# Optimization experiments

Measured on AMD Instinct MI355X. Metric: run time of the kernel, lower is better.

The kernel has to match this reference:

```python
import jax, jax.numpy as jnp
from jax import lax
import numpy as np
import math

T, B, F = 512, 256, 256  # num_steps, batch, input_size == hidden_size
H = F


def setup_inputs() -> dict:
    key = jax.random.key(0)
    ks = jax.random.split(key, 20)
    stdv = 1.0 / math.sqrt(H)

    def u(k, n):
        return jax.random.uniform(k, (n,), jnp.float32, -stdv, stdv)

    X = jax.random.normal(ks[0], (T, B, F), jnp.float32)
    Mask = (jax.random.uniform(ks[1], (T, B, F)) < 0.7).astype(jnp.float32)
    Delta = jax.random.uniform(ks[2], (T, B, F), jnp.float32)

    return {
        "X": X, "Mask": Mask, "Delta": Delta,
        "x_mean": u(ks[3], F),
        "w_dg_x": u(ks[4], F), "b_dg_x": u(ks[5], F),
        "w_dg_h": u(ks[6], H), "b_dg_h": u(ks[7], H),
        "w_xz": u(ks[8], F), "u_hz": u(ks[9], H), "b_z": u(ks[10], H),
        "w_xr": u(ks[11], F), "u_hr": u(ks[12], H), "b_r": u(ks[13], H),
        "w_xh": u(ks[14], F), "u_hh": u(ks[15], H), "v_mh": u(ks[16], F),
        "b_h": u(ks[17], H),
    }


def reference(X, Mask, Delta, x_mean, w_dg_x, b_dg_x, w_dg_h, b_dg_h,
              w_xz, u_hz, b_z, w_xr, u_hr, b_r, w_xh, u_hh, v_mh, b_h):
    batch = X.shape[1]

    def step(h, inp):
        x, m, d = inp  # each [B, F]
        gamma_x = jnp.exp(-jnp.maximum(0.0, w_dg_x * d + b_dg_x))
        gamma_h = jnp.exp(-jnp.maximum(0.0, w_dg_h * d + b_dg_h))
        x = m * x + (1.0 - m) * (gamma_x * x + (1.0 - gamma_x) * x_mean)
        h = gamma_h * h
        z = jax.nn.sigmoid(w_xz * x + u_hz * h + b_z)
        r = jax.nn.sigmoid(w_xr * x + u_hr * h + b_r)
        h_tilde = jnp.tanh(w_xh * x + u_hh * (r * h) + v_mh * m + b_h)
        h = (1.0 - z) * h + z * h_tilde
        return h, h

    h0 = jnp.zeros((batch, H), X.dtype)
    _, hs = lax.scan(step, h0, (X, Mask, Delta))  # hs: [T, B, H]
    hidden_states = jnp.transpose(hs, (1, 0, 2))  # [B, T, H]
    return hidden_states, hidden_states[:, -1, :]
```

## Files before the change

### kernel.cpp

```cpp
#include <hip/hip_runtime.h>
#include <math.h>


#define TT 512
#define BB 256
#define FF 256
#define BF (BB * FF)
#define CH 8
#define NCH (TT / CH)

__device__ __forceinline__ float fast_sigmoid(float x) {
    return __builtin_amdgcn_rcpf(1.0f + __expf(-x));
}
__device__ __forceinline__ float fast_tanh(float x) {
    return fmaf(-2.0f, __builtin_amdgcn_rcpf(1.0f + __expf(2.0f * x)), 1.0f);
}

__global__ __launch_bounds__(512) void grud_kernel(
    const float* __restrict__ X, const float* __restrict__ Mask,
    const float* __restrict__ Delta,
    const float* __restrict__ x_mean,
    const float* __restrict__ w_dg_x, const float* __restrict__ b_dg_x,
    const float* __restrict__ w_dg_h, const float* __restrict__ b_dg_h,
    const float* __restrict__ w_xz, const float* __restrict__ u_hz,
    const float* __restrict__ b_z,
    const float* __restrict__ w_xr, const float* __restrict__ u_hr,
    const float* __restrict__ b_r,
    const float* __restrict__ w_xh, const float* __restrict__ u_hh,
    const float* __restrict__ v_mh, const float* __restrict__ b_h,
    float* __restrict__ out)
{
    __shared__ float lds[2][3][CH][FF];

    const int tid = threadIdx.x;
    const int blk = blockIdx.x;

    if (tid >= 256) {
        const int j = tid - 256;
        const float* srcs[3] = { X     + (size_t)blk * FF,
                                 Mask  + (size_t)blk * FF,
                                 Delta + (size_t)blk * FF };

        {
            #pragma unroll
            for (int arr = 0; arr < 3; ++arr) {
                const float* s = srcs[arr];
                #pragma unroll
                for (int i2 = 0; i2 < 2; ++i2) {
                    const int rem  = i2 * 256 + j;
                    const int step = rem >> 6;
                    const int f4   = (rem & 63) << 2;
                    *(float4*)&lds[0][arr][step][f4] =
                        *(const float4*)(s + (size_t)step * BF + f4);
                }
            }
        }
        __syncthreads();

        for (int k = 0; k < NCH; ++k) {
            if (k + 1 < NCH) {
                const int bufi = (k + 1) & 1;
                const int t0   = (k + 1) * CH;
                #pragma unroll
                for (int arr = 0; arr < 3; ++arr) {
                    const float* s = srcs[arr];
                    #pragma unroll
                    for (int i2 = 0; i2 < 2; ++i2) {
                        const int rem  = i2 * 256 + j;
                        const int step = rem >> 6;
                        const int f4   = (rem & 63) << 2;
                        *(float4*)&lds[bufi][arr][step][f4] =
                            *(const float4*)(s + (size_t)(t0 + step) * BF + f4);
                    }
                }
            }
            __syncthreads();
        }
    } else {
        const int f = tid;
        const float xm  = x_mean[f];
        const float wdx = w_dg_x[f], bdx = b_dg_x[f];
        const float wdh = w_dg_h[f], bdh = b_dg_h[f];
        const float wxz = w_xz[f],   uhz = u_hz[f], bz = b_z[f];
        const float wxr = w_xr[f],   uhr = u_hr[f], br = b_r[f];
        const float wxh = w_xh[f],   uhh = u_hh[f];
        const float vmh = v_mh[f],   bh  = b_h[f];

        float h = 0.0f;
        __syncthreads();

        for (int k = 0; k < NCH; ++k) {
            const int cb = k & 1;
            float* op = out + ((size_t)blk * TT + (size_t)k * CH) * FF + f;
            #pragma unroll
            for (int s = 0; s < CH; ++s) {
                float x = lds[cb][0][s][f];
                float m = lds[cb][1][s][f];
                float d = lds[cb][2][s][f];

                float gx = __expf(-fmaxf(0.0f, fmaf(wdx, d, bdx)));
                float gh = __expf(-fmaxf(0.0f, fmaf(wdh, d, bdh)));
                float xhat = fmaf(gx, x, (1.0f - gx) * xm);
                x = fmaf(m, x, (1.0f - m) * xhat);
                h = gh * h;
                float z  = fast_sigmoid(fmaf(wxz, x, fmaf(uhz, h, bz)));
                float r  = fast_sigmoid(fmaf(wxr, x, fmaf(uhr, h, br)));
                float ht = fast_tanh(fmaf(wxh, x, fmaf(uhh, r * h, fmaf(vmh, m, bh))));
                h = fmaf(z, ht - h, h);
                op[s * FF] = h;
            }
            __syncthreads();
        }

        out[(size_t)BB * TT * FF + (size_t)blk * FF + f] = h;
    }
}

extern "C" void kernel_launch(void* const* d_in, const int* in_sizes, int n_in,
                              void* d_out, int out_size, void* d_ws, size_t ws_size,
                              hipStream_t stream) {
    const float* X      = (const float*)d_in[0];
    const float* Mask   = (const float*)d_in[1];
    const float* Delta  = (const float*)d_in[2];
    const float* x_mean = (const float*)d_in[3];
    const float* w_dg_x = (const float*)d_in[4];
    const float* b_dg_x = (const float*)d_in[5];
    const float* w_dg_h = (const float*)d_in[6];
    const float* b_dg_h = (const float*)d_in[7];
    const float* w_xz   = (const float*)d_in[8];
    const float* u_hz   = (const float*)d_in[9];
    const float* b_z    = (const float*)d_in[10];
    const float* w_xr   = (const float*)d_in[11];
    const float* u_hr   = (const float*)d_in[12];
    const float* b_r    = (const float*)d_in[13];
    const float* w_xh   = (const float*)d_in[14];
    const float* u_hh   = (const float*)d_in[15];
    const float* v_mh   = (const float*)d_in[16];
    const float* b_h    = (const float*)d_in[17];
    float* out = (float*)d_out;

    grud_kernel<<<BB, 512, 0, stream>>>(
        X, Mask, Delta, x_mean, w_dg_x, b_dg_x, w_dg_h, b_dg_h,
        w_xz, u_hz, b_z, w_xr, u_hr, b_r, w_xh, u_hh, v_mh, b_h, out);
}
```

Measured before the change: 417.6 us.

## Replace block barriers with LDS flag-based producer/consumer ring and register prefetch

Replaces the double-buffered __syncthreads handshake with a 4-slot LDS ring, where per-slot produced/consumed counters are updated by wave-leader atomics and polled with s_sleep. Producer waves keep four chunks of global loads in flight in registers before storing them into LDS. The chunk size drops to 4 steps. The consumer math is also reordered so the x-dependent gate terms are computed off the h dependency chain. The goal is to decouple loader and compute waves and hide memory latency, at the cost of spin-wait overhead and reliance on correct memory ordering of LDS flags.

New measurement: 507.0 us. 21.4% more time.

```diff
diff --git a/kernel.cpp b/kernel.cpp
--- a/kernel.cpp
+++ b/kernel.cpp
@@ -6,8 +6,9 @@
 #define BB 256
 #define FF 256
 #define BF (BB * FF)
-#define CH 8
+#define CH 4
 #define NCH (TT / CH)
+#define DSLOTS 4
 
 __device__ __forceinline__ float fast_sigmoid(float x) {
     return __builtin_amdgcn_rcpf(1.0f + __expf(-x));
@@ -30,51 +31,55 @@
     const float* __restrict__ v_mh, const float* __restrict__ b_h,
     float* __restrict__ out)
 {
-    __shared__ float lds[2][3][CH][FF];
+    __shared__ float ring[DSLOTS][3][CH][FF];
+    __shared__ int produced[DSLOTS];
+    __shared__ int consumed[DSLOTS];
 
     const int tid = threadIdx.x;
     const int blk = blockIdx.x;
 
+    if (tid < DSLOTS) { produced[tid] = 0; consumed[tid] = 0; }
+    __syncthreads();
+
     if (tid >= 256) {
-        const int j = tid - 256;
-        const float* srcs[3] = { X     + (size_t)blk * FF,
-                                 Mask  + (size_t)blk * FF,
-                                 Delta + (size_t)blk * FF };
+        const int j   = tid - 256;
+        const int stp = j >> 6;
+        const int f4  = (j & 63) << 2;
+        const size_t eoff = (size_t)blk * FF + (size_t)stp * BF + f4;
+        const float* sX = X     + eoff;
+        const float* sM = Mask  + eoff;
+        const float* sD = Delta + eoff;
+        const int lane0 = ((tid & 63) == 0);
 
-        {
-            #pragma unroll
-            for (int arr = 0; arr < 3; ++arr) {
-                const float* s = srcs[arr];
-                #pragma unroll
-                for (int i2 = 0; i2 < 2; ++i2) {
-                    const int rem  = i2 * 256 + j;
-                    const int step = rem >> 6;
-                    const int f4   = (rem & 63) << 2;
-                    *(float4*)&lds[0][arr][step][f4] =
-                        *(const float4*)(s + (size_t)step * BF + f4);
-                }
-            }
-        }
-        __syncthreads();
+        float4 R0[3], R1[3], R2[3], R3[3];
 
-        for (int k = 0; k < NCH; ++k) {
-            if (k + 1 < NCH) {
-                const int bufi = (k + 1) & 1;
-                const int t0   = (k + 1) * CH;
-                #pragma unroll
-                for (int arr = 0; arr < 3; ++arr) {
-                    const float* s = srcs[arr];
-                    #pragma unroll
-                    for (int i2 = 0; i2 < 2; ++i2) {
-                        const int rem  = i2 * 256 + j;
-                        const int step = rem >> 6;
-                        const int f4   = (rem & 63) << 2;
-                        *(float4*)&lds[bufi][arr][step][f4] =
-                            *(const float4*)(s + (size_t)(t0 + step) * BF + f4);
-                    }
-                }
-            }
-            __syncthreads();
+        auto issue = [&](int chunk, float4 (&R)[3]) {
+            const size_t o = (size_t)chunk * (CH * BF);
+            R[0] = *(const float4*)(sX + o);
+            R[1] = *(const float4*)(sM + o);
+            R[2] = *(const float4*)(sD + o);
+        };
+        auto process = [&](int k, float4 (&R)[3]) {
+            const int s = k & (DSLOTS - 1);
+            const int g = k >> 2;
+            volatile int* cons = consumed + s;
+            const int tgt = 4 * g;
+            while (*cons < tgt) __builtin_amdgcn_s_sleep(1);
+            asm volatile("" ::: "memory");
+            *(float4*)&ring[s][0][stp][f4] = R[0];
+            *(float4*)&ring[s][1][stp][f4] = R[1];
+            *(float4*)&ring[s][2][stp][f4] = R[2];
+            asm volatile("s_waitcnt lgkmcnt(0)" ::: "memory");
+            if (lane0) atomicAdd(&produced[s], 1);
+            if (k + 4 < NCH) issue(k + 4, R);
+        };
+
+        issue(0, R0); issue(1, R1); issue(2, R2); issue(3, R3);
+        for (int kb = 0; kb < NCH; kb += 4) {
+            process(kb + 0, R0);
+            process(kb + 1, R1);
+            process(kb + 2, R2);
+            process(kb + 3, R3);
         }
     } else {
         const int f = tid;
@@ -85,31 +90,42 @@
         const float wxr = w_xr[f],   uhr = u_hr[f], br = b_r[f];
         const float wxh = w_xh[f],   uhh = u_hh[f];
         const float vmh = v_mh[f],   bh  = b_h[f];
+        const int lane0 = ((tid & 63) == 0);
 
         float h = 0.0f;
-        __syncthreads();
+        float* ob = out + (size_t)blk * (TT * FF) + f;
 
         for (int k = 0; k < NCH; ++k) {
-            const int cb = k & 1;
-            float* op = out + ((size_t)blk * TT + (size_t)k * CH) * FF + f;
+            const int s = k & (DSLOTS - 1);
+            const int g = k >> 2;
+            volatile int* prod = produced + s;
+            const int tgt = 4 * (g + 1);
+            while (*prod < tgt) __builtin_amdgcn_s_sleep(1);
+            asm volatile("" ::: "memory");
+
+            float* op = ob + (size_t)(k * CH) * FF;
             #pragma unroll
-            for (int s = 0; s < CH; ++s) {
-                float x = lds[cb][0][s][f];
-                float m = lds[cb][1][s][f];
-                float d = lds[cb][2][s][f];
+            for (int st = 0; st < CH; ++st) {
+                float x = ring[s][0][st][f];
+                float m = ring[s][1][st][f];
+                float d = ring[s][2][st][f];
 
                 float gx = __expf(-fmaxf(0.0f, fmaf(wdx, d, bdx)));
                 float gh = __expf(-fmaxf(0.0f, fmaf(wdh, d, bdh)));
-                float xhat = fmaf(gx, x, (1.0f - gx) * xm);
-                x = fmaf(m, x, (1.0f - m) * xhat);
-                h = gh * h;
-                float z  = fast_sigmoid(fmaf(wxz, x, fmaf(uhz, h, bz)));
-                float r  = fast_sigmoid(fmaf(wxr, x, fmaf(uhr, h, br)));
-                float ht = fast_tanh(fmaf(wxh, x, fmaf(uhh, r * h, fmaf(vmh, m, bh))));
-                h = fmaf(z, ht - h, h);
-                op[s * FF] = h;
+                float xv = fmaf(gx, x, (1.0f - gx) * xm);
+                xv = fmaf(m, x, (1.0f - m) * xv);
+                float az = fmaf(wxz, xv, bz);
+                float ar = fmaf(wxr, xv, br);
+                float ah = fmaf(wxh, xv, fmaf(vmh, m, bh));
+                float u  = gh * h;
+                float z  = fast_sigmoid(fmaf(uhz, u, az));
+                float r  = fast_sigmoid(fmaf(uhr, u, ar));
+                float ht = fast_tanh(fmaf(uhh, r * u, ah));
+                h = fmaf(z, ht - u, u);
+                op[st * FF] = h;
             }
-            __syncthreads();
+            asm volatile("s_waitcnt lgkmcnt(0)" ::: "memory");
+            if (lane0) atomicAdd(&consumed[s], 1);
         }
 
         out[(size_t)BB * TT * FF + (size_t)blk * FF + f] = h;
```
